# Optimization experiments

Measured on AMD Instinct MI355X. Metric: run time of the kernel, lower is better.

Reference implementation:

```python
import jax, jax.numpy as jnp
import numpy as np

U_A = 110.0  # upper bound of feature norm (init kwarg u_a)


def setup_inputs() -> dict:
    key = jax.random.key(0)
    k1, k2, k3, k4 = jax.random.split(key, 4)
    B, C = 256, 100000
    cos_theta = jax.random.normal(k1, (B, C), dtype=jnp.float32)
    cos_theta_m = jax.random.normal(k2, (B, C), dtype=jnp.float32)
    # feature norms in [l_a, u_a] = [10, 110]
    x_norm = 10.0 + 100.0 * jax.random.uniform(k3, (B,), dtype=jnp.float32)
    target = jax.random.randint(k4, (B,), 0, C, dtype=jnp.int32)
    return {"cos_theta": cos_theta, "cos_theta_m": cos_theta_m,
            "x_norm": x_norm, "target": target}


def reference(cos_theta, cos_theta_m, x_norm, target):
    B, C = cos_theta.shape
    # one-hot scatter: one_hot[i, target[i]] = 1 (world_size=1 -> full class dim)
    one_hot = jax.nn.one_hot(target, C, dtype=cos_theta.dtype)  # [B, C]
    # loss_G regularizer: g = x_norm / u_a^2 + 1 / x_norm
    loss_g = jnp.mean(x_norm / (U_A * U_A) + 1.0 / x_norm)
    # margin blend: use cos_theta_m at the target class, cos_theta elsewhere
    output = one_hot * cos_theta_m + (1.0 - one_hot) * cos_theta  # [B, C]
    # cross-entropy with stable log-softmax (distributed LSE collapses to this)
    logp = jax.nn.log_softmax(output, axis=-1)
    loss = -jnp.take_along_axis(logp, target[:, None], axis=-1)[:, 0]  # [B]
    return (loss.mean(), loss_g, one_hot)
```

## Files before the change

### kernel.cpp

```cpp
#include <hip/hip_runtime.h>


#define UA2_INV (1.0f / 12100.0f)
#define SEG 8
#define SEG_SHIFT 3

typedef float v4f __attribute__((ext_vector_type(4)));
typedef float v2f __attribute__((ext_vector_type(2)));

__device__ __forceinline__ void fix_target(float4& v, int c, int t4, int kt4,
                                           float ctm_t) {
    if (c == t4) {
        v.x = (kt4 == 0) ? ctm_t : v.x;
        v.y = (kt4 == 1) ? ctm_t : v.y;
        v.z = (kt4 == 2) ? ctm_t : v.z;
        v.w = (kt4 == 3) ? ctm_t : v.w;
    }
}

__device__ __forceinline__ float exp_sum4(const float4& v) {
    return (__expf(v.x) + __expf(v.y)) + (__expf(v.z) + __expf(v.w));
}

__global__ __launch_bounds__(256) void magloss_part_kernel(
    const float* __restrict__ ct,
    const float* __restrict__ ctm,
    const int*   __restrict__ target,
    float*       __restrict__ onehot,
    float*       __restrict__ part,
    float*       __restrict__ ctmt,
    int C)
{
    const int bid = blockIdx.x;
    const int row = bid >> SEG_SHIFT;
    const int seg = bid & (SEG - 1);
    const size_t base = (size_t)row * (size_t)C;
    const int t = target[row];
    const float ctm_t = ctm[base + (size_t)t];

    if (seg == 0 && threadIdx.x == 0) ctmt[row] = ctm_t;

    float* oh = onehot + base;
    v4f* __restrict__ oh4 = (v4f*)(oh + 2);
    const int K   = (C - 2) >> 2;
    const int ups = (K + SEG - 1) >> SEG_SHIFT;
    const int u0 = seg * ups;
    const int u1 = min(u0 + ups, K);
    const int ut = (t >= 2) ? ((t - 2) >> 2) : -1;
    const int kt = (t - 2) & 3;

    for (int u = u0 + (int)threadIdx.x; u < u1; u += 256) {
        v4f z = {0.f, 0.f, 0.f, 0.f};
        if (u == ut) {
            z.x = (kt == 0) ? 1.f : 0.f;
            z.y = (kt == 1) ? 1.f : 0.f;
            z.z = (kt == 2) ? 1.f : 0.f;
            z.w = (kt == 3) ? 1.f : 0.f;
        }
        oh4[u] = z;
    }
    if (seg == 0 && threadIdx.x == 1) {
        v2f f;
        f.x = (t == 0) ? 1.f : 0.f;
        f.y = (t == 1) ? 1.f : 0.f;
        *(v2f*)oh = f;
    }
    if (seg == SEG - 1) {
        for (int j = 2 + 4 * K + (int)threadIdx.x; j < C; j += 256)
            oh[j] = (j == t) ? 1.f : 0.f;
    }

    const int nchunk = C >> 2;
    const int cps = (nchunk + SEG - 1) >> SEG_SHIFT;
    const int c0 = seg * cps;
    const int c1 = min(c0 + cps, nchunk);
    const int t4  = t >> 2;
    const int kt4 = t & 3;

    const float4* __restrict__ ct4 = (const float4*)(ct + base);

    float s0 = 0.f, s1 = 0.f, s2 = 0.f, s3 = 0.f;
    int c = c0 + (int)threadIdx.x;
    for (; c + 768 < c1; c += 1024) {
        float4 a = ct4[c];
        float4 b = ct4[c + 256];
        float4 d = ct4[c + 512];
        float4 e = ct4[c + 768];
        fix_target(a, c,       t4, kt4, ctm_t);
        fix_target(b, c + 256, t4, kt4, ctm_t);
        fix_target(d, c + 512, t4, kt4, ctm_t);
        fix_target(e, c + 768, t4, kt4, ctm_t);
        s0 += exp_sum4(a);
        s1 += exp_sum4(b);
        s2 += exp_sum4(d);
        s3 += exp_sum4(e);
    }
    for (; c < c1; c += 256) {
        float4 a = ct4[c];
        fix_target(a, c, t4, kt4, ctm_t);
        s0 += exp_sum4(a);
    }
    if (seg == SEG - 1) {
        for (int j = (nchunk << 2) + (int)threadIdx.x; j < C; j += 256) {
            const float v = (j == t) ? ctm_t : ct[base + (size_t)j];
            s1 += __expf(v);
        }
    }

    float s = (s0 + s1) + (s2 + s3);

    #pragma unroll
    for (int off = 32; off; off >>= 1)
        s += __shfl_xor(s, off);

    __shared__ float ss[4];
    const int wave = threadIdx.x >> 6;
    const int lane = threadIdx.x & 63;
    if (lane == 0) ss[wave] = s;
    __syncthreads();

    if (threadIdx.x == 0)
        part[bid] = (ss[0] + ss[1]) + (ss[2] + ss[3]);
}

__global__ __launch_bounds__(256) void magloss_finalize_kernel(
    const float* __restrict__ part,
    const float* __restrict__ ctmt,
    const float* __restrict__ x_norm,
    float*       __restrict__ out,
    int B)
{
    const int i = threadIdx.x;
    float l = 0.f, g = 0.f;
    for (int r = i; r < B; r += 256) {
        const float* p = part + (r << SEG_SHIFT);
        float S = 0.f;
        #pragma unroll
        for (int sgi = 0; sgi < SEG; ++sgi) S += p[sgi];
        l += __logf(S) - ctmt[r];
        const float xn = x_norm[r];
        g += xn * UA2_INV + 1.0f / xn;
    }
    #pragma unroll
    for (int off = 32; off; off >>= 1) {
        l += __shfl_xor(l, off);
        g += __shfl_xor(g, off);
    }
    __shared__ float sl[4], sg[4];
    const int wave = i >> 6;
    const int lane = i & 63;
    if (lane == 0) { sl[wave] = l; sg[wave] = g; }
    __syncthreads();
    if (i == 0) {
        float L = 0.f, G = 0.f;
        #pragma unroll
        for (int w = 0; w < 4; ++w) { L += sl[w]; G += sg[w]; }
        out[0] = L / (float)B;
        out[1] = G / (float)B;
    }
}

extern "C" void kernel_launch(void* const* d_in, const int* in_sizes, int n_in,
                              void* d_out, int out_size, void* d_ws, size_t ws_size,
                              hipStream_t stream) {
    const float* ct  = (const float*)d_in[0];
    const float* ctm = (const float*)d_in[1];
    const float* xn  = (const float*)d_in[2];
    const int*   tg  = (const int*)d_in[3];

    const int B = in_sizes[2];
    const int C = in_sizes[0] / B;

    float* out  = (float*)d_out;
    float* part = (float*)d_ws;
    float* ctmt = part + B * SEG;

    magloss_part_kernel<<<B * SEG, 256, 0, stream>>>(ct, ctm, tg, out + 2, part, ctmt, C);
    magloss_finalize_kernel<<<1, 256, 0, stream>>>(part, ctmt, xn, out, B);
}
```

Baseline: 33.88 us.

## Split one-hot zero-fill into separate aligned fill kernel, scatter ones afterwards

Moves the one-hot output zeroing out of the exp/sum kernel into a dedicated grid-stride kernel that writes the whole output buffer with aligned 16-byte stores. The main kernel then only sets the single target element to one per row. The aim is to get fully aligned vector stores (the previous layout was offset by two floats) and to let the reduction kernel be purely read-bound. The cost is an extra kernel launch, and the separate write pass loses any overlap between writes and reads inside one kernel.

Result: slower. 39.27 us (+15.9%).

```diff
diff --git a/kernel.cpp b/kernel.cpp
--- a/kernel.cpp
+++ b/kernel.cpp
@@ -6,7 +6,6 @@
 #define SEG_SHIFT 3
 
 typedef float v4f __attribute__((ext_vector_type(4)));
-typedef float v2f __attribute__((ext_vector_type(2)));
 
 __device__ __forceinline__ void fix_target(float4& v, int c, int t4, int kt4,
                                            float ctm_t) {
@@ -22,7 +21,21 @@
     return (__expf(v.x) + __expf(v.y)) + (__expf(v.z) + __expf(v.w));
 }
 
-__global__ __launch_bounds__(256) void magloss_part_kernel(
+__global__ __launch_bounds__(256) void magloss_fill_kernel(
+    v4f* __restrict__ out4,
+    int n4,
+    float* __restrict__ tail,
+    int ntail)
+{
+    const v4f z = {0.f, 0.f, 0.f, 0.f};
+    const int stride = gridDim.x * 256;
+    for (int i = blockIdx.x * 256 + (int)threadIdx.x; i < n4; i += stride)
+        out4[i] = z;
+    const int k = blockIdx.x * 256 + (int)threadIdx.x;
+    if (k < ntail) tail[k] = 0.f;
+}
+
+__global__ __launch_bounds__(256) void magloss_exp_kernel(
     const float* __restrict__ ct,
     const float* __restrict__ ctm,
     const int*   __restrict__ target,
@@ -38,36 +51,9 @@
     const int t = target[row];
     const float ctm_t = ctm[base + (size_t)t];
 
-    if (seg == 0 && threadIdx.x == 0) ctmt[row] = ctm_t;
-
-    float* oh = onehot + base;
-    v4f* __restrict__ oh4 = (v4f*)(oh + 2);
-    const int K   = (C - 2) >> 2;
-    const int ups = (K + SEG - 1) >> SEG_SHIFT;
-    const int u0 = seg * ups;
-    const int u1 = min(u0 + ups, K);
-    const int ut = (t >= 2) ? ((t - 2) >> 2) : -1;
-    const int kt = (t - 2) & 3;
-
-    for (int u = u0 + (int)threadIdx.x; u < u1; u += 256) {
-        v4f z = {0.f, 0.f, 0.f, 0.f};
-        if (u == ut) {
-            z.x = (kt == 0) ? 1.f : 0.f;
-            z.y = (kt == 1) ? 1.f : 0.f;
-            z.z = (kt == 2) ? 1.f : 0.f;
-            z.w = (kt == 3) ? 1.f : 0.f;
-        }
-        oh4[u] = z;
-    }
-    if (seg == 0 && threadIdx.x == 1) {
-        v2f f;
-        f.x = (t == 0) ? 1.f : 0.f;
-        f.y = (t == 1) ? 1.f : 0.f;
-        *(v2f*)oh = f;
-    }
-    if (seg == SEG - 1) {
-        for (int j = 2 + 4 * K + (int)threadIdx.x; j < C; j += 256)
-            oh[j] = (j == t) ? 1.f : 0.f;
+    if (seg == 0 && threadIdx.x == 0) {
+        ctmt[row] = ctm_t;
+        onehot[base + (size_t)t] = 1.0f;
     }
 
     const int nchunk = C >> 2;
@@ -175,6 +161,12 @@
     float* part = (float*)d_ws;
     float* ctmt = part + B * SEG;
 
-    magloss_part_kernel<<<B * SEG, 256, 0, stream>>>(ct, ctm, tg, out + 2, part, ctmt, C);
+    const int n4    = out_size >> 2;
+    const int ntail = out_size - (n4 << 2);
+
+    magloss_fill_kernel<<<2048, 256, 0, stream>>>((v4f*)out, n4,
+                                                  out + ((size_t)n4 << 2), ntail);
+    magloss_exp_kernel<<<B * SEG, 256, 0, stream>>>(ct, ctm, tg, out + 2,
+                                                    part, ctmt, C);
     magloss_finalize_kernel<<<1, 256, 0, stream>>>(part, ctmt, xn, out, B);
 }
```
